# Kernel tuning notes

Measured on AMD Instinct MI355X. Metric: run time of the kernel, lower is better.

## Reference

```python
import jax, jax.numpy as jnp
import numpy as np

NUM_HEADS_Q = 32
NUM_HEADS_KV = 8
HEAD_DIM = 128
THETA = 500000.0
B = 2
S = 1024


def _precompute_freqs(head_dim, seq_len, theta):
    half = head_dim // 2
    freqs = 1.0 / theta ** (jnp.arange(half, dtype=jnp.float32) / half)
    positions = jnp.arange(seq_len, dtype=jnp.float32)
    angles = positions[:, None] * freqs[None, :]  # (S, half)
    return jnp.cos(angles), jnp.sin(angles)


def _apply_rope(x, cos, sin):
    # x: (B, H, S, D); cos/sin: (S, D//2)
    half = x.shape[-1] // 2
    x1, x2 = x[..., :half], x[..., half:]
    c = cos[None, None]
    s = sin[None, None]
    return jnp.concatenate([x1 * c - x2 * s, x1 * s + x2 * c], axis=-1)


def setup_inputs() -> dict:
    key = jax.random.key(0)
    kq, kk, kv = jax.random.split(key, 3)
    q = jax.random.normal(kq, (B, 1, S, NUM_HEADS_Q * HEAD_DIM), dtype=jnp.float32)
    k = jax.random.normal(kk, (B, 1, S, NUM_HEADS_KV * HEAD_DIM), dtype=jnp.float32)
    v = jax.random.normal(kv, (B, 1, S, NUM_HEADS_KV * HEAD_DIM), dtype=jnp.float32)
    return {"q": q, "k": k, "v": v}


def reference(q, k, v) -> jnp.ndarray:
    D = HEAD_DIM
    gqa = NUM_HEADS_Q // NUM_HEADS_KV
    scale = 1.0 / np.sqrt(D).astype(np.float32)

    # (B,1,S,H*D) -> (B,H,S,D)
    qh = q.reshape(B, S, NUM_HEADS_Q, D).transpose(0, 2, 1, 3)
    kh = k.reshape(B, S, NUM_HEADS_KV, D).transpose(0, 2, 1, 3)
    vh = v.reshape(B, S, NUM_HEADS_KV, D).transpose(0, 2, 1, 3)

    cos, sin = _precompute_freqs(D, S, THETA)
    qh = _apply_rope(qh, cos, sin)
    kh = _apply_rope(kh, cos, sin)

    if gqa > 1:
        kh = jnp.repeat(kh, gqa, axis=1)   # (B, Hq, S, D)
        vh = jnp.repeat(vh, gqa, axis=1)

    scores = jnp.einsum('bhqd,bhkd->bhqk', qh, kh) * scale  # (B, Hq, S, S)
    causal = jnp.tril(jnp.ones((S, S), dtype=bool))
    scores = jnp.where(causal[None, None], scores, -jnp.inf)
    weights = jax.nn.softmax(scores, axis=-1)
    attn = jnp.einsum('bhqk,bhkd->bhqd', weights, vh)  # (B, Hq, S, D)
    out = attn.transpose(0, 2, 1, 3).reshape(B, 1, S, NUM_HEADS_Q * D)
    return out
```

## Files before the change

### kernel.cpp

```cpp
#include <hip/hip_runtime.h>
#include <math.h>

typedef __attribute__((ext_vector_type(4))) float f32x4;
typedef __attribute__((ext_vector_type(16))) float f32x16;
typedef __attribute__((ext_vector_type(8))) short bf16x8;

namespace {
constexpr int kB = 2;
constexpr int kS = 1024;
constexpr int kD = 128;
constexpr float kScale = 0.08838834764831845f;
constexpr float kLog2e = 1.4426950408889634f;
constexpr float kFreqC = 0.20503692777194262f;
constexpr int kKPad = 136;
constexpr int kVPad = 72;

constexpr size_t kTabOff = 0;
constexpr size_t kKOff = 512 * 1024;
constexpr size_t kVOff = kKOff + 4194304;
constexpr size_t kWsNeed = kVOff + 4194304;
}

#define VMCNT(n) asm volatile("s_waitcnt vmcnt(" #n ")" ::: "memory")

__device__ inline short f2bf(float f) {
  union { float f; unsigned u; } c{f};
  unsigned r = c.u + 0x7fffu + ((c.u >> 16) & 1u);
  return (short)(r >> 16);
}

__device__ inline unsigned pkbf(float a, float b) {
  unsigned r;
  asm("v_cvt_pk_bf16_f32 %0, %1, %2" : "=v"(r) : "v"(a), "v"(b));
  return r;
}

__device__ inline void gload16(const void* g, void* l) {
  __builtin_amdgcn_global_load_lds(
      (const __attribute__((address_space(1))) void*)g,
      (__attribute__((address_space(3))) void*)l, 16, 0, 0);
}

__global__ __launch_bounds__(256) void rope_table_k(float2* __restrict__ tab) {
  int t = blockIdx.x * 256 + threadIdx.x;
  int pos = t >> 6, j = t & 63;
  float ang = (float)pos * expf(-(float)j * kFreqC);
  float sn, cs;
  sincosf(ang, &sn, &cs);
  tab[t] = make_float2(cs, sn);
}

__global__ __launch_bounds__(256) void prep_k(
    const float* __restrict__ k, const float* __restrict__ v,
    short* __restrict__ Kp, short* __restrict__ Vp, float2* __restrict__ tab) {
  __shared__ float Tl[64][68];
  int bid = blockIdx.x;
  if (bid < 1024) {
    int t2 = bid * 256 + threadIdx.x;
    int j = (t2 & 15) * 4;
    int h = (t2 >> 4) & 7;
    int s = (t2 >> 7) & 1023;
    int b = t2 >> 17;
    size_t sidx = ((size_t)b * 1024 + s) * 1024 + h * 128 + j;
    size_t didx = (((size_t)b * 8 + h) * 1024 + s) * 128 + j;
    float4 x1 = *(const float4*)&k[sidx];
    float4 x2 = *(const float4*)&k[sidx + 64];
    float cs[4], sn[4];
#pragma unroll
    for (int jj = 0; jj < 4; ++jj) {
      float ang = (float)s * expf(-(float)(j + jj) * kFreqC);
      sincosf(ang, &sn[jj], &cs[jj]);
    }
    short4 y1, y2;
    y1.x = f2bf(x1.x * cs[0] - x2.x * sn[0]);
    y2.x = f2bf(x1.x * sn[0] + x2.x * cs[0]);
    y1.y = f2bf(x1.y * cs[1] - x2.y * sn[1]);
    y2.y = f2bf(x1.y * sn[1] + x2.y * cs[1]);
    y1.z = f2bf(x1.z * cs[2] - x2.z * sn[2]);
    y2.z = f2bf(x1.z * sn[2] + x2.z * cs[2]);
    y1.w = f2bf(x1.w * cs[3] - x2.w * sn[3]);
    y2.w = f2bf(x1.w * sn[3] + x2.w * cs[3]);
    *(short4*)&Kp[didx] = y1;
    *(short4*)&Kp[didx + 64] = y2;
  } else if (bid < 1536) {
    int blk = bid - 1024;
    int bh = blk >> 5;
    int rem = blk & 31;
    int s0 = (rem >> 1) * 64;
    int d0 = (rem & 1) * 64;
    int t = threadIdx.x;
#pragma unroll
    for (int i = 0; i < 4; ++i) {
      int srow = i * 16 + (t >> 4);
      int scol = (t & 15) * 4;
      float4 x = *(const float4*)&v[((size_t)(bh >> 3) * 1024 + s0 + srow) * 1024 +
                                    (bh & 7) * 128 + d0 + scol];
      *(float4*)&Tl[srow][scol] = x;
    }
    __syncthreads();
#pragma unroll
    for (int i = 0; i < 4; ++i) {
      int drow = i * 16 + (t >> 4);
      int sq = (t & 15) * 4;
      short4 y;
      y.x = f2bf(Tl[sq + 0][drow]);
      y.y = f2bf(Tl[sq + 1][drow]);
      y.z = f2bf(Tl[sq + 2][drow]);
      y.w = f2bf(Tl[sq + 3][drow]);
      *(short4*)&Vp[((size_t)bh * 128 + d0 + drow) * 1024 + s0 + sq] = y;
    }
  } else {
    int t = (bid - 1536) * 256 + threadIdx.x;
    int pos = t >> 6, j = t & 63;
    float ang = (float)pos * expf(-(float)j * kFreqC);
    float sn, cs;
    sincosf(ang, &sn, &cs);
    tab[t] = make_float2(cs, sn);
  }
}

__global__ __launch_bounds__(256, 2) void attnks_k(
    const float* __restrict__ q, const short* __restrict__ Kp,
    const short* __restrict__ Vp, const float2* __restrict__ tab,
    float* __restrict__ out) {
  __shared__ char KV[2][32768];

  const int tid = threadIdx.x;
  const int w = tid >> 6;
  const int lane = tid & 63;
  const int l31 = lane & 31;
  const int hi5 = lane >> 5;
  const int qsub = w & 1;
  const int kh = w >> 1;
  const int fb = blockIdx.x;
  const int hq = blockIdx.y;
  const int b = blockIdx.z;
  const int hkv = hq >> 2;

  const char* Kh = (const char*)(Kp + ((size_t)b * 8 + hkv) * 1024 * 128);
  const char* Vh = (const char*)(Vp + ((size_t)b * 8 + hkv) * 128 * 1024);
  float* Lf = (float*)KV;

#define STAGE(k0_, bufi_)                                                     \
  {                                                                           \
    char* Kd = KV[bufi_];                                                     \
    char* Vd = KV[bufi_] + 16384;                                             \
    _Pragma("unroll") for (int ii = 0; ii < 4; ++ii) {                        \
      int i = w * 4 + ii;                                                     \
      int row = i * 4 + (lane >> 4);                                          \
      int srcb = ((k0_) + row) * 256 + (((lane & 15) * 16) ^ ((row & 7) << 4)); \
      gload16(Kh + srcb, Kd + i * 1024);                                      \
    }                                                                         \
    _Pragma("unroll") for (int ii = 0; ii < 4; ++ii) {                        \
      int i = w * 4 + ii;                                                     \
      int d = i * 8 + (lane >> 3);                                            \
      int srcb = d * 2048 + (k0_) * 2 + (((lane & 7) * 16) ^ ((d & 7) << 4)); \
      gload16(Vh + srcb, Vd + i * 1024);                                      \
    }                                                                         \
  }

  for (int half = 0; half < 2; ++half) {
    const int qt = (half ^ (b & 1)) ? (15 - fb) : fb;
    const int q0 = qt * 64;
    const int nk = qt + 1;
    const int qrow = q0 + qsub * 32 + l31;

    STAGE(0, 0);

    const float* qp = q + ((size_t)b * 1024 + qrow) * 4096 + hq * 128;
    const float2* tp = tab + (size_t)qrow * 64;
    bf16x8 qB[8];
#pragma unroll
    for (int g = 0; g < 4; ++g) {
      int jb = g * 16 + hi5 * 8;
      float4 x1a = *(const float4*)&qp[jb];
      float4 x1b = *(const float4*)&qp[jb + 4];
      float4 x2a = *(const float4*)&qp[jb + 64];
      float4 x2b = *(const float4*)&qp[jb + 68];
      float4 t0 = *(const float4*)&tp[jb];
      float4 t1 = *(const float4*)&tp[jb + 2];
      float4 t2 = *(const float4*)&tp[jb + 4];
      float4 t3 = *(const float4*)&tp[jb + 6];
      float lo[8], hb[8];
      lo[0] = (x1a.x * t0.x - x2a.x * t0.y) * kScale;
      hb[0] = (x1a.x * t0.y + x2a.x * t0.x) * kScale;
      lo[1] = (x1a.y * t0.z - x2a.y * t0.w) * kScale;
      hb[1] = (x1a.y * t0.w + x2a.y * t0.z) * kScale;
      lo[2] = (x1a.z * t1.x - x2a.z * t1.y) * kScale;
      hb[2] = (x1a.z * t1.y + x2a.z * t1.x) * kScale;
      lo[3] = (x1a.w * t1.z - x2a.w * t1.w) * kScale;
      hb[3] = (x1a.w * t1.w + x2a.w * t1.z) * kScale;
      lo[4] = (x1b.x * t2.x - x2b.x * t2.y) * kScale;
      hb[4] = (x1b.x * t2.y + x2b.x * t2.x) * kScale;
      lo[5] = (x1b.y * t2.z - x2b.y * t2.w) * kScale;
      hb[5] = (x1b.y * t2.w + x2b.y * t2.z) * kScale;
      lo[6] = (x1b.z * t3.x - x2b.z * t3.y) * kScale;
      hb[6] = (x1b.z * t3.y + x2b.z * t3.x) * kScale;
      lo[7] = (x1b.w * t3.z - x2b.w * t3.w) * kScale;
      hb[7] = (x1b.w * t3.w + x2b.w * t3.z) * kScale;
      union { unsigned u[4]; bf16x8 v; } A, C;
#pragma unroll
      for (int ww = 0; ww < 4; ++ww) {
        A.u[ww] = pkbf(lo[2 * ww], lo[2 * ww + 1]);
        C.u[ww] = pkbf(hb[2 * ww], hb[2 * ww + 1]);
      }
      qB[g] = A.v;
      qB[g + 4] = C.v;
    }

    float m = -3e38f, l = 0.f;
    f32x16 acc[4];
#pragma unroll
    for (int dt = 0; dt < 4; ++dt)
#pragma unroll
      for (int e = 0; e < 16; ++e) acc[dt][e] = 0.f;

    int buf = 0;
    for (int t = 0; t < nk; ++t) {
      if (t < nk - 1) {
        STAGE((t + 1) * 64, buf ^ 1);
        VMCNT(8);
      } else {
        VMCNT(0);
      }
      __builtin_amdgcn_sched_barrier(0);
      __builtin_amdgcn_s_barrier();
      __builtin_amdgcn_sched_barrier(0);

      if (!(t == qt && qsub == 0 && kh == 1)) {
        const char* Ks = KV[buf];
        const char* Vt = KV[buf] + 16384;

        f32x16 sc;
#pragma unroll
        for (int e = 0; e < 16; ++e) sc[e] = 0.f;
        const int krow = kh * 32 + l31;
        const int kswz = (l31 & 7) << 4;
        __builtin_amdgcn_s_setprio(1);
#pragma unroll
        for (int c = 0; c < 8; ++c) {
          bf16x8 kf = *(const bf16x8*)(Ks + krow * 256 +
                                       ((c * 32 + hi5 * 16) ^ kswz));
          sc = __builtin_amdgcn_mfma_f32_32x32x16_bf16(kf, qB[c], sc, 0, 0, 0);
        }
        __builtin_amdgcn_s_setprio(0);

        if (t == qt && qsub == kh) {
          int kb = t * 64 + kh * 32 + 4 * hi5;
#pragma unroll
          for (int r = 0; r < 16; ++r)
            if (kb + (r & 3) + 8 * (r >> 2) > qrow) sc[r] = -3e38f;
        }

        float tv = -3e38f;
#pragma unroll
        for (int r = 0; r < 16; ++r) tv = fmaxf(tv, sc[r]);
        tv = fmaxf(tv, __shfl_xor(tv, 32));
        if (!__all(tv <= m + 8.f)) {
          float mn = fmaxf(m, tv);
          float al = exp2f((m - mn) * kLog2e);
          m = mn;
          l *= al;
#pragma unroll
          for (int r = 0; r < 16; ++r) {
            float alr = __shfl(al, (r & 3) + 8 * (r >> 2) + 4 * hi5);
            acc[0][r] *= alr;
            acc[1][r] *= alr;
            acc[2][r] *= alr;
            acc[3][r] *= alr;
          }
        }
        float rs = 0.f;
#pragma unroll
        for (int r = 0; r < 16; ++r) {
          sc[r] = exp2f((sc[r] - m) * kLog2e);
          rs += sc[r];
        }
        rs += __shfl_xor(rs, 32);
        l += rs;

        __builtin_amdgcn_s_setprio(1);
#define PV_CHUNK(CI)                                                          \
        {                                                                     \
          unsigned p0 = pkbf(sc[8 * (CI) + 0], sc[8 * (CI) + 1]);             \
          unsigned p1 = pkbf(sc[8 * (CI) + 2], sc[8 * (CI) + 3]);             \
          unsigned p2 = pkbf(sc[8 * (CI) + 4], sc[8 * (CI) + 5]);             \
          unsigned p3 = pkbf(sc[8 * (CI) + 6], sc[8 * (CI) + 7]);             \
          asm("v_permlane32_swap_b32 %0, %1" : "+v"(p0), "+v"(p2));           \
          asm("v_permlane32_swap_b32 %0, %1" : "+v"(p1), "+v"(p3));           \
          union { unsigned u[4]; bf16x8 v; } pa;                              \
          pa.u[0] = p0; pa.u[1] = p1; pa.u[2] = p2; pa.u[3] = p3;             \
          int ko = (kh * 2 + (CI)) * 32 + hi5 * 16;                           \
          _Pragma("unroll") for (int dt = 0; dt < 4; ++dt) {                  \
            int d = dt * 32 + l31;                                            \
            bf16x8 vf = *(const bf16x8*)(Vt + d * 128 + (ko ^ ((d & 7) << 4))); \
            acc[dt] = __builtin_amdgcn_mfma_f32_32x32x16_bf16(pa.v, vf,       \
                                                              acc[dt], 0, 0, 0); \
          }                                                                   \
        }
        PV_CHUNK(0)
        PV_CHUNK(1)
#undef PV_CHUNK
        __builtin_amdgcn_s_setprio(0);
      }

      __builtin_amdgcn_sched_barrier(0);
      __builtin_amdgcn_s_barrier();
      __builtin_amdgcn_sched_barrier(0);
      buf ^= 1;
    }

    const int mbase = qsub * 4224;
    if (kh == 1) {
#pragma unroll
      for (int dt = 0; dt < 4; ++dt)
#pragma unroll
        for (int c4 = 0; c4 < 4; ++c4) {
          f32x4 v4 = {acc[dt][c4 * 4], acc[dt][c4 * 4 + 1],
                      acc[dt][c4 * 4 + 2], acc[dt][c4 * 4 + 3]};
          *(f32x4*)&Lf[mbase + (dt * 4 + c4) * 256 + lane * 4] = v4;
        }
      Lf[mbase + 4096 + lane] = m;
      Lf[mbase + 4160 + lane] = l;
    }
    __syncthreads();
    if (kh == 0) {
      float m2 = Lf[mbase + 4096 + lane];
      float l2 = Lf[mbase + 4160 + lane];
      float mm = fmaxf(m, m2);
      float a1 = exp2f((m - mm) * kLog2e);
      float a2 = exp2f((m2 - mm) * kLog2e);
      float lt = l * a1 + l2 * a2;
      float linv = 1.f / lt;
      const size_t obase =
          ((size_t)b * 1024 + q0 + qsub * 32) * 4096 + (size_t)hq * 128;
#pragma unroll
      for (int r = 0; r < 16; ++r) {
        int rq = (r & 3) + 8 * (r >> 2) + 4 * hi5;
        float a1r = __shfl(a1, rq);
        float a2r = __shfl(a2, rq);
        float ilr = __shfl(linv, rq);
        float* orow = out + obase + (size_t)rq * 4096 + l31;
#pragma unroll
        for (int dt = 0; dt < 4; ++dt) {
          float o2 = Lf[mbase + (dt * 4 + (r >> 2)) * 256 + lane * 4 + (r & 3)];
          orow[dt * 32] = (acc[dt][r] * a1r + o2 * a2r) * ilr;
        }
      }
    }
    __syncthreads();
  }
#undef STAGE
}

template <bool USE_TAB>
__global__ __launch_bounds__(256) void attn_k(
    const float* __restrict__ q, const float* __restrict__ k,
    const float* __restrict__ v, const float2* __restrict__ tab,
    float* __restrict__ out) {
  __shared__ short Ksf[64][kKPad];
  __shared__ short Vtf[kD][kVPad];
  __shared__ short Qbuf[64 * kKPad];
  const int tid = threadIdx.x;
  const int w = tid >> 6;
  const int lane = tid & 63;
  const int lrow = lane & 15;
  const int lk8 = (lane >> 4) * 8;
  const int qt = (int)gridDim.x - 1 - (int)blockIdx.x;
  const int hq = blockIdx.y;
  const int b = blockIdx.z;
  const int hkv = hq >> 2;
  const int q0 = qt * 64;
  const float* qb = q + (size_t)b * kS * 4096 + hq * kD;
  const float* kb = k + (size_t)b * kS * 1024 + hkv * kD;
  const float* vb = v + (size_t)b * kS * 1024 + hkv * kD;
#pragma unroll
  for (int it = 0; it < 16; ++it) {
    int pi = tid + it * 256;
    int row = pi >> 6, j = pi & 63;
    int pos = q0 + row;
    float x1 = qb[(size_t)pos * 4096 + j];
    float x2 = qb[(size_t)pos * 4096 + j + 64];
    float c, s;
    if (USE_TAB) { float2 t2 = tab[(pos << 6) + j]; c = t2.x; s = t2.y; }
    else { float ang = (float)pos * __expf(-(float)j * kFreqC); __sincosf(ang, &s, &c); }
    Qbuf[row * kKPad + j]      = f2bf((x1 * c - x2 * s) * kScale);
    Qbuf[row * kKPad + j + 64] = f2bf((x1 * s + x2 * c) * kScale);
  }
  __syncthreads();
  bf16x8 qf[4];
#pragma unroll
  for (int d = 0; d < 4; ++d)
    qf[d] = *(const bf16x8*)&Qbuf[(w * 16 + lrow) * kKPad + d * 32 + lk8];
  __syncthreads();
  short* myP = Qbuf + w * 16 * kVPad;
  float mS[4] = {-3e38f, -3e38f, -3e38f, -3e38f};
  float lS[4] = {0.f, 0.f, 0.f, 0.f};
  f32x4 acc[8];
#pragma unroll
  for (int dt = 0; dt < 8; ++dt) acc[dt] = f32x4{0.f, 0.f, 0.f, 0.f};
  for (int kt = 0; kt <= qt; ++kt) {
    const int k0 = kt * 64;
#pragma unroll
    for (int it = 0; it < 16; ++it) {
      int pi = tid + it * 256;
      int row = pi >> 6, j = pi & 63;
      int pos = k0 + row;
      float x1 = kb[(size_t)pos * 1024 + j];
      float x2 = kb[(size_t)pos * 1024 + j + 64];
      float c, s;
      if (USE_TAB) { float2 t2 = tab[(pos << 6) + j]; c = t2.x; s = t2.y; }
      else { float ang = (float)pos * __expf(-(float)j * kFreqC); __sincosf(ang, &s, &c); }
      Ksf[row][j]      = f2bf(x1 * c - x2 * s);
      Ksf[row][j + 64] = f2bf(x1 * s + x2 * c);
    }
#pragma unroll
    for (int it = 0; it < 8; ++it) {
      int f = (tid + it * 256) * 4;
      int row = f >> 7, col = f & 127;
      const float4 v4 = *(const float4*)(vb + (size_t)(k0 + row) * 1024 + col);
      Vtf[col + 0][row] = f2bf(v4.x);
      Vtf[col + 1][row] = f2bf(v4.y);
      Vtf[col + 2][row] = f2bf(v4.z);
      Vtf[col + 3][row] = f2bf(v4.w);
    }
    __syncthreads();
    f32x4 sc[4];
#pragma unroll
    for (int ct = 0; ct < 4; ++ct) {
      sc[ct] = f32x4{0.f, 0.f, 0.f, 0.f};
#pragma unroll
      for (int d = 0; d < 4; ++d) {
        bf16x8 kf = *(const bf16x8*)&Ksf[ct * 16 + lrow][d * 32 + lk8];
        sc[ct] = __builtin_amdgcn_mfma_f32_16x16x32_bf16(qf[d], kf, sc[ct], 0, 0, 0);
      }
    }
    if (kt == qt) {
#pragma unroll
      for (int ct = 0; ct < 4; ++ct) {
        int col = ct * 16 + lrow;
#pragma unroll
        for (int r = 0; r < 4; ++r) {
          int row = w * 16 + (lane >> 4) * 4 + r;
          if (col > row) sc[ct][r] = -3e38f;
        }
      }
    }
#pragma unroll
    for (int r = 0; r < 4; ++r) {
      float t = fmaxf(fmaxf(sc[0][r], sc[1][r]), fmaxf(sc[2][r], sc[3][r]));
      t = fmaxf(t, __shfl_xor(t, 1));
      t = fmaxf(t, __shfl_xor(t, 2));
      t = fmaxf(t, __shfl_xor(t, 4));
      t = fmaxf(t, __shfl_xor(t, 8));
      float mn = fmaxf(mS[r], t);
      float al = exp2f((mS[r] - mn) * kLog2e);
      float rs = 0.f;
#pragma unroll
      for (int ct = 0; ct < 4; ++ct) {
        float p = exp2f((sc[ct][r] - mn) * kLog2e);
        sc[ct][r] = p;
        rs += p;
      }
      rs += __shfl_xor(rs, 1);
      rs += __shfl_xor(rs, 2);
      rs += __shfl_xor(rs, 4);
      rs += __shfl_xor(rs, 8);
      lS[r] = lS[r] * al + rs;
      mS[r] = mn;
#pragma unroll
      for (int dt = 0; dt < 8; ++dt) acc[dt][r] *= al;
    }
#pragma unroll
    for (int ct = 0; ct < 4; ++ct)
#pragma unroll
      for (int r = 0; r < 4; ++r)
        myP[((lane >> 4) * 4 + r) * kVPad + ct * 16 + lrow] = f2bf(sc[ct][r]);
#pragma unroll
    for (int ks = 0; ks < 2; ++ks) {
      bf16x8 pf = *(const bf16x8*)&myP[lrow * kVPad + ks * 32 + lk8];
#pragma unroll
      for (int dt = 0; dt < 8; ++dt) {
        bf16x8 vf = *(const bf16x8*)&Vtf[dt * 16 + lrow][ks * 32 + lk8];
        acc[dt] = __builtin_amdgcn_mfma_f32_16x16x32_bf16(pf, vf, acc[dt], 0, 0, 0);
      }
    }
    __syncthreads();
  }
  float il[4];
#pragma unroll
  for (int r = 0; r < 4; ++r) il[r] = 1.f / lS[r];
  float* ob = out + ((size_t)b * kS + q0 + w * 16) * 4096 + hq * kD;
#pragma unroll
  for (int dt = 0; dt < 8; ++dt)
#pragma unroll
    for (int r = 0; r < 4; ++r)
      ob[((lane >> 4) * 4 + r) * 4096 + dt * 16 + lrow] = acc[dt][r] * il[r];
}

extern "C" void kernel_launch(void* const* d_in, const int* in_sizes, int n_in,
                              void* d_out, int out_size, void* d_ws, size_t ws_size,
                              hipStream_t stream) {
  const float* q = (const float*)d_in[0];
  const float* k = (const float*)d_in[1];
  const float* v = (const float*)d_in[2];
  float* out = (float*)d_out;

  if (ws_size >= kWsNeed) {
    float2* tab = (float2*)((char*)d_ws + kTabOff);
    short* Kp = (short*)((char*)d_ws + kKOff);
    short* Vp = (short*)((char*)d_ws + kVOff);
    prep_k<<<1792, 256, 0, stream>>>(k, v, Kp, Vp, tab);
    dim3 grid(8, 32, kB);
    attnks_k<<<grid, 256, 0, stream>>>(q, Kp, Vp, tab, out);
  } else if (ws_size >= 512 * 1024) {
    float2* tab = (float2*)d_ws;
    rope_table_k<<<256, 256, 0, stream>>>(tab);
    dim3 grid(16, 32, kB);
    attn_k<true><<<grid, 256, 0, stream>>>(q, k, v, tab, out);
  } else {
    dim3 grid(16, 32, kB);
    attn_k<false><<<grid, 256, 0, stream>>>(q, k, v, nullptr, out);
  }
}
```

Measured before the change: 59.68 us.

## Load V fragments directly from global in MFMA-ready layout, shrink LDS, one q-tile per block

The prep kernel now stores V in 32-key blocked tiles laid out so each lane can load its PV MFMA operand straight from global/L2, removing V staging through LDS. With LDS halved, occupancy is raised to three blocks per CU and each block handles a single q-tile (grid doubled, longest tiles first) instead of a paired light/heavy tile. K staging now waits with vmcnt(0) and issues the next prefetch after the barrier. The trade-off is that V is read per wave from global memory without LDS reuse, adding latency and L2 traffic, and the K prefetch overlap is reduced.

```diff
diff --git a/kernel.cpp b/kernel.cpp
--- a/kernel.cpp
+++ b/kernel.cpp
@@ -107,7 +107,9 @@
       y.y = f2bf(Tl[sq + 1][drow]);
       y.z = f2bf(Tl[sq + 2][drow]);
       y.w = f2bf(Tl[sq + 3][drow]);
-      *(short4*)&Vp[((size_t)bh * 128 + d0 + drow) * 1024 + s0 + sq] = y;
+      int kb = (s0 + sq) >> 5;
+      int kk = (s0 + sq) & 31;
+      *(short4*)&Vp[(((size_t)bh * 32 + kb) * 128 + d0 + drow) * 32 + kk] = y;
     }
   } else {
     int t = (bid - 1536) * 256 + threadIdx.x;
@@ -119,11 +121,12 @@
   }
 }
 
-__global__ __launch_bounds__(256, 2) void attnks_k(
+__global__ __launch_bounds__(256, 3) void attnv_k(
     const float* __restrict__ q, const short* __restrict__ Kp,
     const short* __restrict__ Vp, const float2* __restrict__ tab,
     float* __restrict__ out) {
-  __shared__ char KV[2][32768];
+  __shared__ char KV[2][16384];
+  __shared__ float Pml[2][128];
 
   const int tid = threadIdx.x;
   const int w = tid >> 6;
@@ -132,225 +135,214 @@
   const int hi5 = lane >> 5;
   const int qsub = w & 1;
   const int kh = w >> 1;
-  const int fb = blockIdx.x;
+  const int qt = 15 - (int)blockIdx.x;
   const int hq = blockIdx.y;
   const int b = blockIdx.z;
   const int hkv = hq >> 2;
+  const int q0 = qt * 64;
+  const int nk = qt + 1;
+  const int qrow = q0 + qsub * 32 + l31;
 
   const char* Kh = (const char*)(Kp + ((size_t)b * 8 + hkv) * 1024 * 128);
-  const char* Vh = (const char*)(Vp + ((size_t)b * 8 + hkv) * 128 * 1024);
-  float* Lf = (float*)KV;
-
-#define STAGE(k0_, bufi_)                                                     \
+  const short* Vh2 = Vp + ((size_t)b * 8 + hkv) * 131072;
+
+#define STAGE_K(k0_, bufi_)                                                   \
   {                                                                           \
     char* Kd = KV[bufi_];                                                     \
-    char* Vd = KV[bufi_] + 16384;                                             \
     _Pragma("unroll") for (int ii = 0; ii < 4; ++ii) {                        \
       int i = w * 4 + ii;                                                     \
       int row = i * 4 + (lane >> 4);                                          \
       int srcb = ((k0_) + row) * 256 + (((lane & 15) * 16) ^ ((row & 7) << 4)); \
       gload16(Kh + srcb, Kd + i * 1024);                                      \
     }                                                                         \
-    _Pragma("unroll") for (int ii = 0; ii < 4; ++ii) {                        \
-      int i = w * 4 + ii;                                                     \
-      int d = i * 8 + (lane >> 3);                                            \
-      int srcb = d * 2048 + (k0_) * 2 + (((lane & 7) * 16) ^ ((d & 7) << 4)); \
-      gload16(Vh + srcb, Vd + i * 1024);                                      \
-    }                                                                         \
-  }
-
-  for (int half = 0; half < 2; ++half) {
-    const int qt = (half ^ (b & 1)) ? (15 - fb) : fb;
-    const int q0 = qt * 64;
-    const int nk = qt + 1;
-    const int qrow = q0 + qsub * 32 + l31;
-
-    STAGE(0, 0);
-
-    const float* qp = q + ((size_t)b * 1024 + qrow) * 4096 + hq * 128;
-    const float2* tp = tab + (size_t)qrow * 64;
-    bf16x8 qB[8];
-#pragma unroll
-    for (int g = 0; g < 4; ++g) {
-      int jb = g * 16 + hi5 * 8;
-      float4 x1a = *(const float4*)&qp[jb];
-      float4 x1b = *(const float4*)&qp[jb + 4];
-      float4 x2a = *(const float4*)&qp[jb + 64];
-      float4 x2b = *(const float4*)&qp[jb + 68];
-      float4 t0 = *(const float4*)&tp[jb];
-      float4 t1 = *(const float4*)&tp[jb + 2];
-      float4 t2 = *(const float4*)&tp[jb + 4];
-      float4 t3 = *(const float4*)&tp[jb + 6];
-      float lo[8], hb[8];
-      lo[0] = (x1a.x * t0.x - x2a.x * t0.y) * kScale;
-      hb[0] = (x1a.x * t0.y + x2a.x * t0.x) * kScale;
-      lo[1] = (x1a.y * t0.z - x2a.y * t0.w) * kScale;
-      hb[1] = (x1a.y * t0.w + x2a.y * t0.z) * kScale;
-      lo[2] = (x1a.z * t1.x - x2a.z * t1.y) * kScale;
-      hb[2] = (x1a.z * t1.y + x2a.z * t1.x) * kScale;
-      lo[3] = (x1a.w * t1.z - x2a.w * t1.w) * kScale;
-      hb[3] = (x1a.w * t1.w + x2a.w * t1.z) * kScale;
-      lo[4] = (x1b.x * t2.x - x2b.x * t2.y) * kScale;
-      hb[4] = (x1b.x * t2.y + x2b.x * t2.x) * kScale;
-      lo[5] = (x1b.y * t2.z - x2b.y * t2.w) * kScale;
-      hb[5] = (x1b.y * t2.w + x2b.y * t2.z) * kScale;
-      lo[6] = (x1b.z * t3.x - x2b.z * t3.y) * kScale;
-      hb[6] = (x1b.z * t3.y + x2b.z * t3.x) * kScale;
-      lo[7] = (x1b.w * t3.z - x2b.w * t3.w) * kScale;
-      hb[7] = (x1b.w * t3.w + x2b.w * t3.z) * kScale;
-      union { unsigned u[4]; bf16x8 v; } A, C;
-#pragma unroll
-      for (int ww = 0; ww < 4; ++ww) {
-        A.u[ww] = pkbf(lo[2 * ww], lo[2 * ww + 1]);
-        C.u[ww] = pkbf(hb[2 * ww], hb[2 * ww + 1]);
-      }
-      qB[g] = A.v;
-      qB[g + 4] = C.v;
-    }
-
-    float m = -3e38f, l = 0.f;
-    f32x16 acc[4];
+  }
+
+  STAGE_K(0, 0);
+
+  const float* qp = q + ((size_t)b * 1024 + qrow) * 4096 + hq * 128;
+  const float2* tp = tab + (size_t)qrow * 64;
+  bf16x8 qB[8];
+#pragma unroll
+  for (int g = 0; g < 4; ++g) {
+    int jb = g * 16 + hi5 * 8;
+    float4 x1a = *(const float4*)&qp[jb];
+    float4 x1b = *(const float4*)&qp[jb + 4];
+    float4 x2a = *(const float4*)&qp[jb + 64];
+    float4 x2b = *(const float4*)&qp[jb + 68];
+    float4 t0 = *(const float4*)&tp[jb];
+    float4 t1 = *(const float4*)&tp[jb + 2];
+    float4 t2 = *(const float4*)&tp[jb + 4];
+    float4 t3 = *(const float4*)&tp[jb + 6];
+    float lo[8], hb[8];
+    lo[0] = (x1a.x * t0.x - x2a.x * t0.y) * kScale;
+    hb[0] = (x1a.x * t0.y + x2a.x * t0.x) * kScale;
+    lo[1] = (x1a.y * t0.z - x2a.y * t0.w) * kScale;
+    hb[1] = (x1a.y * t0.w + x2a.y * t0.z) * kScale;
+    lo[2] = (x1a.z * t1.x - x2a.z * t1.y) * kScale;
+    hb[2] = (x1a.z * t1.y + x2a.z * t1.x) * kScale;
+    lo[3] = (x1a.w * t1.z - x2a.w * t1.w) * kScale;
+    hb[3] = (x1a.w * t1.w + x2a.w * t1.z) * kScale;
+    lo[4] = (x1b.x * t2.x - x2b.x * t2.y) * kScale;
+    hb[4] = (x1b.x * t2.y + x2b.x * t2.x) * kScale;
+    lo[5] = (x1b.y * t2.z - x2b.y * t2.w) * kScale;
+    hb[5] = (x1b.y * t2.w + x2b.y * t2.z) * kScale;
+    lo[6] = (x1b.z * t3.x - x2b.z * t3.y) * kScale;
+    hb[6] = (x1b.z * t3.y + x2b.z * t3.x) * kScale;
+    lo[7] = (x1b.w * t3.z - x2b.w * t3.w) * kScale;
+    hb[7] = (x1b.w * t3.w + x2b.w * t3.z) * kScale;
+    union { unsigned u[4]; bf16x8 v; } A, C;
+#pragma unroll
+    for (int ww = 0; ww < 4; ++ww) {
+      A.u[ww] = pkbf(lo[2 * ww], lo[2 * ww + 1]);
+      C.u[ww] = pkbf(hb[2 * ww], hb[2 * ww + 1]);
+    }
+    qB[g] = A.v;
+    qB[g + 4] = C.v;
+  }
+
+  float m = -3e38f, l = 0.f;
+  f32x16 acc[4];
+#pragma unroll
+  for (int dt = 0; dt < 4; ++dt)
+#pragma unroll
+    for (int e = 0; e < 16; ++e) acc[dt][e] = 0.f;
+
+  int buf = 0;
+  for (int t = 0; t < nk; ++t) {
+    VMCNT(0);
+    __builtin_amdgcn_sched_barrier(0);
+    __builtin_amdgcn_s_barrier();
+    __builtin_amdgcn_sched_barrier(0);
+
+    if (t < nk - 1) STAGE_K((t + 1) * 64, buf ^ 1);
+
+    if (!(t == qt && qsub == 0 && kh == 1)) {
+      const short* Vkb = Vh2 + (size_t)(t * 2 + kh) * 4096;
+      bf16x8 vf[8];
+#pragma unroll
+      for (int dt = 0; dt < 4; ++dt)
+#pragma unroll
+        for (int s = 0; s < 2; ++s)
+          vf[dt * 2 + s] =
+              *(const bf16x8*)(Vkb + (dt * 32 + l31) * 32 + s * 16 + hi5 * 8);
+
+      const char* Ks = KV[buf];
+
+      f32x16 sc;
+#pragma unroll
+      for (int e = 0; e < 16; ++e) sc[e] = 0.f;
+      const int krow = kh * 32 + l31;
+      const int kswz = (l31 & 7) << 4;
+      __builtin_amdgcn_s_setprio(1);
+#pragma unroll
+      for (int c = 0; c < 8; ++c) {
+        bf16x8 kf = *(const bf16x8*)(Ks + krow * 256 +
+                                     ((c * 32 + hi5 * 16) ^ kswz));
+        sc = __builtin_amdgcn_mfma_f32_32x32x16_bf16(kf, qB[c], sc, 0, 0, 0);
+      }
+      __builtin_amdgcn_s_setprio(0);
+
+      if (t == qt && qsub == kh) {
+        int kb = t * 64 + kh * 32 + 4 * hi5;
+#pragma unroll
+        for (int r = 0; r < 16; ++r)
+          if (kb + (r & 3) + 8 * (r >> 2) > qrow) sc[r] = -3e38f;
+      }
+
+      float tv = -3e38f;
+#pragma unroll
+      for (int r = 0; r < 16; ++r) tv = fmaxf(tv, sc[r]);
+      tv = fmaxf(tv, __shfl_xor(tv, 32));
+      if (!__all(tv <= m + 8.f)) {
+        float mn = fmaxf(m, tv);
+        float al = exp2f((m - mn) * kLog2e);
+        m = mn;
+        l *= al;
+#pragma unroll
+        for (int r = 0; r < 16; ++r) {
+          float alr = __shfl(al, (r & 3) + 8 * (r >> 2) + 4 * hi5);
+          acc[0][r] *= alr;
+          acc[1][r] *= alr;
+          acc[2][r] *= alr;
+          acc[3][r] *= alr;
+        }
+      }
+      float rs = 0.f;
+#pragma unroll
+      for (int r = 0; r < 16; ++r) {
+        sc[r] = exp2f((sc[r] - m) * kLog2e);
+        rs += sc[r];
+      }
+      rs += __shfl_xor(rs, 32);
+      l += rs;
+
+      __builtin_amdgcn_s_setprio(1);
+#define PV_CHUNK(CI)                                                          \
+      {                                                                       \
+        unsigned p0 = pkbf(sc[8 * (CI) + 0], sc[8 * (CI) + 1]);               \
+        unsigned p1 = pkbf(sc[8 * (CI) + 2], sc[8 * (CI) + 3]);               \
+        unsigned p2 = pkbf(sc[8 * (CI) + 4], sc[8 * (CI) + 5]);               \
+        unsigned p3 = pkbf(sc[8 * (CI) + 6], sc[8 * (CI) + 7]);               \
+        asm("v_permlane32_swap_b32 %0, %1" : "+v"(p0), "+v"(p2));             \
+        asm("v_permlane32_swap_b32 %0, %1" : "+v"(p1), "+v"(p3));             \
+        union { unsigned u[4]; bf16x8 v; } pa;                                \
+        pa.u[0] = p0; pa.u[1] = p1; pa.u[2] = p2; pa.u[3] = p3;               \
+        _Pragma("unroll") for (int dt = 0; dt < 4; ++dt) {                    \
+          acc[dt] = __builtin_amdgcn_mfma_f32_32x32x16_bf16(                  \
+              pa.v, vf[dt * 2 + (CI)], acc[dt], 0, 0, 0);                     \
+        }                                                                     \
+      }
+      PV_CHUNK(0)
+      PV_CHUNK(1)
+#undef PV_CHUNK
+      __builtin_amdgcn_s_setprio(0);
+    }
+
+    __builtin_amdgcn_sched_barrier(0);
+    __builtin_amdgcn_s_barrier();
+    __builtin_amdgcn_sched_barrier(0);
+    buf ^= 1;
+  }
+
+  float* Lq = (float*)KV[qsub];
+  if (kh == 1) {
 #pragma unroll
     for (int dt = 0; dt < 4; ++dt)
 #pragma unroll
-      for (int e = 0; e < 16; ++e) acc[dt][e] = 0.f;
-
-    int buf = 0;
-    for (int t = 0; t < nk; ++t) {
-      if (t < nk - 1) {
-        STAGE((t + 1) * 64, buf ^ 1);
-        VMCNT(8);
-      } else {
-        VMCNT(0);
-      }
-      __builtin_amdgcn_sched_barrier(0);
-      __builtin_amdgcn_s_barrier();
-      __builtin_amdgcn_sched_barrier(0);
-
-      if (!(t == qt && qsub == 0 && kh == 1)) {
-        const char* Ks = KV[buf];
-        const char* Vt = KV[buf] + 16384;
-
-        f32x16 sc;
-#pragma unroll
-        for (int e = 0; e < 16; ++e) sc[e] = 0.f;
-        const int krow = kh * 32 + l31;
-        const int kswz = (l31 & 7) << 4;
-        __builtin_amdgcn_s_setprio(1);
-#pragma unroll
-        for (int c = 0; c < 8; ++c) {
-          bf16x8 kf = *(const bf16x8*)(Ks + krow * 256 +
-                                       ((c * 32 + hi5 * 16) ^ kswz));
-          sc = __builtin_amdgcn_mfma_f32_32x32x16_bf16(kf, qB[c], sc, 0, 0, 0);
-        }
-        __builtin_amdgcn_s_setprio(0);
-
-        if (t == qt && qsub == kh) {
-          int kb = t * 64 + kh * 32 + 4 * hi5;
-#pragma unroll
-          for (int r = 0; r < 16; ++r)
-            if (kb + (r & 3) + 8 * (r >> 2) > qrow) sc[r] = -3e38f;
-        }
-
-        float tv = -3e38f;
-#pragma unroll
-        for (int r = 0; r < 16; ++r) tv = fmaxf(tv, sc[r]);
-        tv = fmaxf(tv, __shfl_xor(tv, 32));
-        if (!__all(tv <= m + 8.f)) {
-          float mn = fmaxf(m, tv);
-          float al = exp2f((m - mn) * kLog2e);
-          m = mn;
-          l *= al;
-#pragma unroll
-          for (int r = 0; r < 16; ++r) {
-            float alr = __shfl(al, (r & 3) + 8 * (r >> 2) + 4 * hi5);
-            acc[0][r] *= alr;
-            acc[1][r] *= alr;
-            acc[2][r] *= alr;
-            acc[3][r] *= alr;
-          }
-        }
-        float rs = 0.f;
-#pragma unroll
-        for (int r = 0; r < 16; ++r) {
-          sc[r] = exp2f((sc[r] - m) * kLog2e);
-          rs += sc[r];
-        }
-        rs += __shfl_xor(rs, 32);
-        l += rs;
-
-        __builtin_amdgcn_s_setprio(1);
-#define PV_CHUNK(CI)                                                          \
-        {                                                                     \
-          unsigned p0 = pkbf(sc[8 * (CI) + 0], sc[8 * (CI) + 1]);             \
-          unsigned p1 = pkbf(sc[8 * (CI) + 2], sc[8 * (CI) + 3]);             \
-          unsigned p2 = pkbf(sc[8 * (CI) + 4], sc[8 * (CI) + 5]);             \
-          unsigned p3 = pkbf(sc[8 * (CI) + 6], sc[8 * (CI) + 7]);             \
-          asm("v_permlane32_swap_b32 %0, %1" : "+v"(p0), "+v"(p2));           \
-          asm("v_permlane32_swap_b32 %0, %1" : "+v"(p1), "+v"(p3));           \
-          union { unsigned u[4]; bf16x8 v; } pa;                              \
-          pa.u[0] = p0; pa.u[1] = p1; pa.u[2] = p2; pa.u[3] = p3;             \
-          int ko = (kh * 2 + (CI)) * 32 + hi5 * 16;                           \
-          _Pragma("unroll") for (int dt = 0; dt < 4; ++dt) {                  \
-            int d = dt * 32 + l31;                                            \
-            bf16x8 vf = *(const bf16x8*)(Vt + d * 128 + (ko ^ ((d & 7) << 4))); \
-            acc[dt] = __builtin_amdgcn_mfma_f32_32x32x16_bf16(pa.v, vf,       \
-                                                              acc[dt], 0, 0, 0); \
-          }                                                                   \
-        }
-        PV_CHUNK(0)
-        PV_CHUNK(1)
-#undef PV_CHUNK
-        __builtin_amdgcn_s_setprio(0);
-      }
-
-      __builtin_amdgcn_sched_barrier(0);
-      __builtin_amdgcn_s_barrier();
-      __builtin_amdgcn_sched_barrier(0);
-      buf ^= 1;
-    }
-
-    const int mbase = qsub * 4224;
-    if (kh == 1) {
-#pragma unroll
-      for (int dt = 0; dt < 4; ++dt)
-#pragma unroll
-        for (int c4 = 0; c4 < 4; ++c4) {
-          f32x4 v4 = {acc[dt][c4 * 4], acc[dt][c4 * 4 + 1],
-                      acc[dt][c4 * 4 + 2], acc[dt][c4 * 4 + 3]};
-          *(f32x4*)&Lf[mbase + (dt * 4 + c4) * 256 + lane * 4] = v4;
-        }
-      Lf[mbase + 4096 + lane] = m;
-      Lf[mbase + 4160 + lane] = l;
-    }
-    __syncthreads();
-    if (kh == 0) {
-      float m2 = Lf[mbase + 4096 + lane];
-      float l2 = Lf[mbase + 4160 + lane];
-      float mm = fmaxf(m, m2);
-      float a1 = exp2f((m - mm) * kLog2e);
-      float a2 = exp2f((m2 - mm) * kLog2e);
-      float lt = l * a1 + l2 * a2;
-      float linv = 1.f / lt;
-      const size_t obase =
-          ((size_t)b * 1024 + q0 + qsub * 32) * 4096 + (size_t)hq * 128;
-#pragma unroll
-      for (int r = 0; r < 16; ++r) {
-        int rq = (r & 3) + 8 * (r >> 2) + 4 * hi5;
-        float a1r = __shfl(a1, rq);
-        float a2r = __shfl(a2, rq);
-        float ilr = __shfl(linv, rq);
-        float* orow = out + obase + (size_t)rq * 4096 + l31;
-#pragma unroll
-        for (int dt = 0; dt < 4; ++dt) {
-          float o2 = Lf[mbase + (dt * 4 + (r >> 2)) * 256 + lane * 4 + (r & 3)];
-          orow[dt * 32] = (acc[dt][r] * a1r + o2 * a2r) * ilr;
-        }
-      }
-    }
-    __syncthreads();
-  }
-#undef STAGE
+      for (int c4 = 0; c4 < 4; ++c4) {
+        f32x4 v4 = {acc[dt][c4 * 4], acc[dt][c4 * 4 + 1],
+                    acc[dt][c4 * 4 + 2], acc[dt][c4 * 4 + 3]};
+        *(f32x4*)&Lq[(dt * 4 + c4) * 256 + lane * 4] = v4;
+      }
+    Pml[qsub][lane] = m;
+    Pml[qsub][64 + lane] = l;
+  }
+  __syncthreads();
+  if (kh == 0) {
+    float m2 = Pml[qsub][lane];
+    float l2 = Pml[qsub][64 + lane];
+    float mm = fmaxf(m, m2);
+    float a1 = exp2f((m - mm) * kLog2e);
+    float a2 = exp2f((m2 - mm) * kLog2e);
+    float lt = l * a1 + l2 * a2;
+    float linv = 1.f / lt;
+    const size_t obase =
+        ((size_t)b * 1024 + q0 + qsub * 32) * 4096 + (size_t)hq * 128;
+#pragma unroll
+    for (int r = 0; r < 16; ++r) {
+      int rq = (r & 3) + 8 * (r >> 2) + 4 * hi5;
+      float a1r = __shfl(a1, rq);
+      float a2r = __shfl(a2, rq);
+      float ilr = __shfl(linv, rq);
+      float* orow = out + obase + (size_t)rq * 4096 + l31;
+#pragma unroll
+      for (int dt = 0; dt < 4; ++dt) {
+        float o2 = Lq[(dt * 4 + (r >> 2)) * 256 + lane * 4 + (r & 3)];
+        orow[dt * 32] = (acc[dt][r] * a1r + o2 * a2r) * ilr;
+      }
+    }
+  }
+#undef STAGE_K
 }
 
 template <bool USE_TAB>
@@ -511,8 +503,8 @@
     short* Kp = (short*)((char*)d_ws + kKOff);
     short* Vp = (short*)((char*)d_ws + kVOff);
     prep_k<<<1792, 256, 0, stream>>>(k, v, Kp, Vp, tab);
-    dim3 grid(8, 32, kB);
-    attnks_k<<<grid, 256, 0, stream>>>(q, Kp, Vp, tab, out);
+    dim3 grid(16, 32, kB);
+    attnv_k<<<grid, 256, 0, stream>>>(q, Kp, Vp, tab, out);
   } else if (ws_size >= 512 * 1024) {
     float2* tab = (float2*)d_ws;
     rope_table_k<<<256, 256, 0, stream>>>(tab);
```

Measured after the change: 155.2 us. +160.0%, slower.
